# Performance work log

Hardware: AMD Instinct MI355X
Metric: run time of the kernel (lower is better)

## Reference

```python
import jax, jax.numpy as jnp
import numpy as np

B, S, D, H, E, F, K = 4, 1024, 1024, 16, 8, 4096, 2
HD = D // H  # 64
EPS = 1e-6


def _rmsnorm(x, w):
    return x * jax.lax.rsqrt(jnp.mean(x * x, axis=-1, keepdims=True) + EPS) * w


def _rope(x, cos, sin):
    # x: [B,S,H,HD]; cos/sin: [S,HD//2]
    b, s, h, hd = x.shape
    x2 = x.reshape(b, s, h, hd // 2, 2)
    xr, xi = x2[..., 0], x2[..., 1]
    c = cos[None, :, None, :]
    sn = sin[None, :, None, :]
    or_ = xr * c - xi * sn
    oi = xr * sn + xi * c
    return jnp.stack([or_, oi], axis=-1).reshape(b, s, h, hd)


def setup_inputs() -> dict:
    key = jax.random.key(0)
    ks = jax.random.split(key, 16)
    sc = 0.02
    # rotary tables (standard LLaMa rope)
    inv = 1.0 / (10000.0 ** (np.arange(0, HD, 2, dtype=np.float32) / HD))
    ang = np.outer(np.arange(S, dtype=np.float32), inv)
    return {
        "q": jax.random.normal(ks[0], (B, S, D), jnp.float32),
        "k": jax.random.normal(ks[1], (B, S, D), jnp.float32),
        "v": jax.random.normal(ks[2], (B, S, D), jnp.float32),
        "freqs_cos": jnp.asarray(np.cos(ang)),
        "freqs_sin": jnp.asarray(np.sin(ang)),
        "att_norm_w": jnp.ones((D,), jnp.float32),
        "ffn_norm_w": jnp.ones((D,), jnp.float32),
        "wq": jax.random.normal(ks[3], (D, D), jnp.float32) * sc,
        "wk": jax.random.normal(ks[4], (D, D), jnp.float32) * sc,
        "wv": jax.random.normal(ks[5], (D, D), jnp.float32) * sc,
        "wo": jax.random.normal(ks[6], (D, D), jnp.float32) * sc,
        "router_w": jax.random.normal(ks[7], (E, D), jnp.float32) * sc,
        "router_b": jnp.zeros((E,), jnp.float32),
        "w1": jax.random.normal(ks[8], (E, F, D), jnp.float32) * sc,
        "w2": jax.random.normal(ks[9], (E, D, F), jnp.float32) * sc,
        "w3": jax.random.normal(ks[10], (E, F, D), jnp.float32) * sc,
        "is_causal": 1,
    }


def _attention(qn, kn, vn, freqs_cos, freqs_sin, wq, wk, wv, wo, is_causal):
    b, s, d = qn.shape
    qh = (qn @ wq.T).reshape(b, s, H, HD)
    kh = (kn @ wk.T).reshape(b, s, H, HD)
    vh = (vn @ wv.T).reshape(b, s, H, HD)
    qh = _rope(qh, freqs_cos, freqs_sin)
    kh = _rope(kh, freqs_cos, freqs_sin)
    scores = jnp.einsum("bqhd,bkhd->bhqk", qh, kh) / jnp.sqrt(jnp.float32(HD))
    if is_causal:
        causal = jnp.tril(jnp.ones((s, s), bool))
        scores = jnp.where(causal[None, None], scores, jnp.float32(-1e30))
    probs = jax.nn.softmax(scores, axis=-1)
    out = jnp.einsum("bhqk,bkhd->bqhd", probs, vh).reshape(b, s, d)
    return out @ wo.T


def _sparse_moe(x, router_w, router_b, w1, w2, w3):
    # x: [B,S,D]
    flat = x.reshape(-1, x.shape[-1])  # [T,D]
    logits = flat @ router_w.T + router_b  # [T,E]
    top_v, top_i = jax.lax.top_k(logits, K)  # eval mode: no noise
    probs = jax.nn.softmax(top_v, axis=-1)  # softmax over -inf-filled == softmax over top-k
    gates = jnp.sum(jax.nn.one_hot(top_i, E, dtype=flat.dtype) * probs[..., None], axis=1)  # [T,E]
    y = jnp.zeros_like(flat)
    for e in range(E):  # fixed small expert loop; gate==0 for unselected tokens (faithful to masked dispatch)
        hgate = jax.nn.silu(flat @ w1[e].T) * (flat @ w3[e].T)  # SwiGLU FFN_LLaMa
        y = y + gates[:, e : e + 1] * (hgate @ w2[e].T)
    return y.reshape(x.shape)


def reference(q, k, v, freqs_cos, freqs_sin, att_norm_w, ffn_norm_w, wq, wk, wv, wo,
              router_w, router_b, w1, w2, w3, is_causal):
    qn = _rmsnorm(q, att_norm_w)
    # self-attention path: k = v = normed q (q.clone())
    h = q + _attention(qn, qn, qn, freqs_cos, freqs_sin, wq, wk, wv, wo, is_causal)
    out = h + _sparse_moe(_rmsnorm(h, ffn_norm_w), router_w, router_b, w1, w2, w3)
    return out
```

## Files before the change

### kernel.cpp

```cpp
#include <hip/hip_runtime.h>
#include <hip/hip_bf16.h>
#include <math.h>

#define NB 4
#define SQ 1024
#define DM 1024
#define NH 16
#define HDm 64
#define NE 8
#define FFd 4096
#define NTOK 4096
#define RTOT 9216
#define EPSF 1e-6f

typedef __attribute__((ext_vector_type(8))) short bf16x8_t;
typedef __attribute__((ext_vector_type(4))) float f32x4_t;
typedef const __attribute__((address_space(1))) void* gas_t;
typedef __attribute__((address_space(3))) void* las_t;

__device__ __forceinline__ float b2f(unsigned short u){
  return __uint_as_float(((unsigned int)u) << 16);
}
__device__ __forceinline__ unsigned short f2b(float f){
  __hip_bfloat16 h = __float2bfloat16(f);
  unsigned short u;
  __builtin_memcpy(&u, &h, 2);
  return u;
}

__global__ __launch_bounds__(256) void convert_k(const float* __restrict__ s,
                                                 unsigned short* __restrict__ d, int n4){
  int i = blockIdx.x*256 + threadIdx.x;
  if (i >= n4) return;
  float4 v = ((const float4*)s)[i];
  ushort4 o; o.x=f2b(v.x); o.y=f2b(v.y); o.z=f2b(v.z); o.w=f2b(v.w);
  ((ushort4*)d)[i] = o;
}

__global__ __launch_bounds__(256) void split_k(const float* __restrict__ s,
                                               unsigned short* __restrict__ hi,
                                               unsigned short* __restrict__ lo, int n4){
  int i = blockIdx.x*256 + threadIdx.x;
  if (i >= n4) return;
  float4 v = ((const float4*)s)[i];
  ushort4 h, l;
  h.x=f2b(v.x); l.x=f2b(v.x - b2f(h.x));
  h.y=f2b(v.y); l.y=f2b(v.y - b2f(h.y));
  h.z=f2b(v.z); l.z=f2b(v.z - b2f(h.z));
  h.w=f2b(v.w); l.w=f2b(v.w - b2f(h.w));
  ((ushort4*)hi)[i] = h;
  ((ushort4*)lo)[i] = l;
}

__global__ __launch_bounds__(256) void rmsnorm_k(const float* __restrict__ x,
                                                 const float* __restrict__ w,
                                                 float* __restrict__ o){
  int row = blockIdx.x; int t = threadIdx.x;
  float4 v = ((const float4*)(x + (size_t)row*DM))[t];
  float ss = v.x*v.x + v.y*v.y + v.z*v.z + v.w*v.w;
  #pragma unroll
  for (int d=32; d; d>>=1) ss += __shfl_down(ss, d, 64);
  __shared__ float red[4];
  int wid = t>>6, ln = t&63;
  if (ln==0) red[wid] = ss;
  __syncthreads();
  float tot = red[0]+red[1]+red[2]+red[3];
  float sc = 1.0f/sqrtf(tot*(1.0f/DM) + EPSF);
  float4 wv = ((const float4*)w)[t];
  float4 ov = { v.x*sc*wv.x, v.y*sc*wv.y, v.z*sc*wv.z, v.w*sc*wv.w };
  ((float4*)(o + (size_t)row*DM))[t] = ov;
}

__global__ __launch_bounds__(256) void rmsnorm_split_k(const float* __restrict__ x,
                                                       const float* __restrict__ w,
                                                       unsigned short* __restrict__ hi,
                                                       unsigned short* __restrict__ lo){
  int row = blockIdx.x; int t = threadIdx.x;
  float4 v = ((const float4*)(x + (size_t)row*DM))[t];
  float ss = v.x*v.x + v.y*v.y + v.z*v.z + v.w*v.w;
  #pragma unroll
  for (int d=32; d; d>>=1) ss += __shfl_down(ss, d, 64);
  __shared__ float red[4];
  int wid = t>>6, ln = t&63;
  if (ln==0) red[wid] = ss;
  __syncthreads();
  float tot = red[0]+red[1]+red[2]+red[3];
  float sc = 1.0f/sqrtf(tot*(1.0f/DM) + EPSF);
  float4 wv = ((const float4*)w)[t];
  float4 ov = { v.x*sc*wv.x, v.y*sc*wv.y, v.z*sc*wv.z, v.w*sc*wv.w };
  ushort4 h, l;
  h.x=f2b(ov.x); l.x=f2b(ov.x - b2f(h.x));
  h.y=f2b(ov.y); l.y=f2b(ov.y - b2f(h.y));
  h.z=f2b(ov.z); l.z=f2b(ov.z - b2f(h.z));
  h.w=f2b(ov.w); l.w=f2b(ov.w - b2f(h.w));
  ((ushort4*)(hi + (size_t)row*DM))[t] = h;
  ((ushort4*)(lo + (size_t)row*DM))[t] = l;
}

__global__ __launch_bounds__(256) void gemm_nt_split(
  const unsigned short* __restrict__ Ah, const unsigned short* __restrict__ Al,
  const unsigned short* __restrict__ Bh0, const unsigned short* __restrict__ Bl0,
  const unsigned short* __restrict__ Bh1, const unsigned short* __restrict__ Bl1,
  const unsigned short* __restrict__ Bh2, const unsigned short* __restrict__ Bl2,
  float* __restrict__ C0, float* __restrict__ C1, float* __restrict__ C2,
  const float* __restrict__ resid, int Kd, int Ncols)
{
  const unsigned short* Bh = (blockIdx.z==0)?Bh0:(blockIdx.z==1)?Bh1:Bh2;
  const unsigned short* Bl = (blockIdx.z==0)?Bl0:(blockIdx.z==1)?Bl1:Bl2;
  float* C = (blockIdx.z==0)?C0:(blockIdx.z==1)?C1:C2;
  __shared__ unsigned short AsH[128*32];
  __shared__ unsigned short AsL[128*32];
  __shared__ unsigned short BsH[128*32];
  __shared__ unsigned short BsL[128*32];
  const int t = threadIdx.x;
  const int w = t>>6, lane = t&63;
  const int wm = w>>1, wn = w&1;
  const int lm = lane&15, fk = (lane>>4)*8;
  const int row0 = blockIdx.y*128, col0 = blockIdx.x*128;
  f32x4_t acc[4][4];
  #pragma unroll
  for (int i=0;i<4;i++)
    #pragma unroll
    for (int j=0;j<4;j++){ f32x4_t z = {0.f,0.f,0.f,0.f}; acc[i][j]=z; }
  for (int k0=0;k0<Kd;k0+=32){
    __syncthreads();
    #pragma unroll
    for (int j=0;j<2;j++){
      const int chunk = j*4 + w;
      const int gt = chunk*64 + lane;
      const int rw_ = gt>>2, kp = (gt&3)*8;
      const size_t aoff = (size_t)(row0+rw_)*Kd + k0 + kp;
      const size_t boff = (size_t)(col0+rw_)*Kd + k0 + kp;
      __builtin_amdgcn_global_load_lds((gas_t)(Ah + aoff), (las_t)(AsH + chunk*512), 16, 0, 0);
      __builtin_amdgcn_global_load_lds((gas_t)(Al + aoff), (las_t)(AsL + chunk*512), 16, 0, 0);
      __builtin_amdgcn_global_load_lds((gas_t)(Bh + boff), (las_t)(BsH + chunk*512), 16, 0, 0);
      __builtin_amdgcn_global_load_lds((gas_t)(Bl + boff), (las_t)(BsL + chunk*512), 16, 0, 0);
    }
    __syncthreads();
    bf16x8_t ah[4], al[4], bh[4], bl[4];
    #pragma unroll
    for (int f=0;f<4;f++){
      const size_t ao = (size_t)(wm*64 + f*16 + lm)*32 + fk;
      const size_t bo = (size_t)(wn*64 + f*16 + lm)*32 + fk;
      ah[f] = *(const bf16x8_t*)(AsH + ao);
      al[f] = *(const bf16x8_t*)(AsL + ao);
      bh[f] = *(const bf16x8_t*)(BsH + bo);
      bl[f] = *(const bf16x8_t*)(BsL + bo);
    }
    #pragma unroll
    for (int i=0;i<4;i++)
      #pragma unroll
      for (int j=0;j<4;j++){
        acc[i][j] = __builtin_amdgcn_mfma_f32_16x16x32_bf16(ah[i], bh[j], acc[i][j], 0, 0, 0);
        acc[i][j] = __builtin_amdgcn_mfma_f32_16x16x32_bf16(al[i], bh[j], acc[i][j], 0, 0, 0);
        acc[i][j] = __builtin_amdgcn_mfma_f32_16x16x32_bf16(ah[i], bl[j], acc[i][j], 0, 0, 0);
      }
  }
  const int rbase = row0 + wm*64 + (lane>>4)*4;
  const int cbase = col0 + wn*64 + lm;
  #pragma unroll
  for (int i=0;i<4;i++)
    #pragma unroll
    for (int j=0;j<4;j++)
      #pragma unroll
      for (int r=0;r<4;r++){
        const size_t idx = (size_t)(rbase + i*16 + r)*Ncols + cbase + j*16;
        float v = acc[i][j][r];
        if (resid) v += resid[idx];
        C[idx] = v;
      }
}

__global__ __launch_bounds__(256) void rope_bf16_k(const float* __restrict__ qh,
  const float* __restrict__ kh, const float* __restrict__ fc, const float* __restrict__ fs,
  unsigned short* __restrict__ qb, unsigned short* __restrict__ kb){
  int idx = blockIdx.x*256 + threadIdx.x;
  if (idx >= NTOK*NH*32) return;
  int i = idx & 31;
  int h = (idx>>5) & (NH-1);
  int n = idx >> 9;
  int s = n & (SQ-1);
  float c = fc[s*32+i], sn = fs[s*32+i];
  size_t base = (size_t)n*DM + h*HDm + 2*i;
  float xr = qh[base], xi = qh[base+1];
  float or_ = (xr*c - xi*sn) * 0.125f;
  float oi  = (xr*sn + xi*c) * 0.125f;
  unsigned int pq = (unsigned int)f2b(or_) | ((unsigned int)f2b(oi) << 16);
  *(unsigned int*)(qb + base) = pq;
  xr = kh[base]; xi = kh[base+1];
  or_ = xr*c - xi*sn; oi = xr*sn + xi*c;
  unsigned int pk = (unsigned int)f2b(or_) | ((unsigned int)f2b(oi) << 16);
  *(unsigned int*)(kb + base) = pk;
}

__global__ __launch_bounds__(256) void vtrans_k(const float* __restrict__ vh,
                                                unsigned short* __restrict__ vT){
  __shared__ unsigned short Lt[64][72];
  const int st = blockIdx.x, bh = blockIdx.y;
  const int b = bh >> 4, h = bh & 15;
  const int t = threadIdx.x;
  const int s0 = st*64;
  const int sr = t >> 2, hq = (t & 3) * 16;
  const float* src = vh + ((size_t)(b*SQ + s0 + sr))*DM + h*HDm + hq;
  #pragma unroll
  for (int i=0;i<4;i++){
    float4 v = *(const float4*)(src + 4*i);
    Lt[hq+4*i+0][sr] = f2b(v.x);
    Lt[hq+4*i+1][sr] = f2b(v.y);
    Lt[hq+4*i+2][sr] = f2b(v.z);
    Lt[hq+4*i+3][sr] = f2b(v.w);
  }
  __syncthreads();
  const int hd = t >> 2, sq = (t & 3) * 16;
  unsigned short* dst = vT + ((size_t)bh*HDm + hd)*SQ + s0 + sq;
  #pragma unroll
  for (int i=0;i<2;i++){
    bf16x8_t x = *(const bf16x8_t*)&Lt[hd][sq + 8*i];
    *(bf16x8_t*)(dst + 8*i) = x;
  }
}

__global__ __launch_bounds__(256) void flash_mfma_k(
  const unsigned short* __restrict__ qb, const unsigned short* __restrict__ kb,
  const unsigned short* __restrict__ vT,
  unsigned short* __restrict__ ctxh, unsigned short* __restrict__ ctxl,
  const int* __restrict__ causp)
{
  __shared__ unsigned short Qs[2*64*32];
  __shared__ unsigned short Ks[2*64*32];
  __shared__ unsigned short Vt[2*64*32];
  __shared__ unsigned short Ps[2*64*32];
  const int qt = blockIdx.x;
  const int bh = blockIdx.y;
  const int b = bh >> 4, h = bh & 15;
  const int t = threadIdx.x;
  const int w = t >> 6, lane = t & 63;
  const int lm = lane & 15, g = lane >> 4, fk = g * 8;
  const int q0 = qt * 64;
  const size_t qkoff = (size_t)b * SQ * DM + (size_t)h * HDm;
  const size_t voff  = ((size_t)bh * HDm) * SQ;

  #pragma unroll
  for (int j=0;j<2;j++){
    const int s = j*4 + w;
    const int c = s >> 2, r0 = (s & 3) * 16;
    const int row = r0 + (lane >> 2), kp = (lane & 3) * 8;
    __builtin_amdgcn_global_load_lds((gas_t)(qb + qkoff + (size_t)(q0+row)*DM + c*32 + kp),
                                     (las_t)(Qs + s*512), 16, 0, 0);
  }
  __syncthreads();
  bf16x8_t aq0 = *(const bf16x8_t*)(Qs + 0*2048 + (w*16+lm)*32 + fk);
  bf16x8_t aq1 = *(const bf16x8_t*)(Qs + 1*2048 + (w*16+lm)*32 + fk);

  const int causal = *causp;
  const int ktmax = causal ? qt : (SQ/64 - 1);
  f32x4_t O[4];
  #pragma unroll
  for (int j=0;j<4;j++){ f32x4_t z={0.f,0.f,0.f,0.f}; O[j]=z; }
  float mrow[4], lrow[4];
  #pragma unroll
  for (int r=0;r<4;r++){ mrow[r] = -3e30f; lrow[r] = 0.f; }

  for (int kt=0; kt<=ktmax; ++kt){
    const int k0 = kt*64;
    __syncthreads();
    #pragma unroll
    for (int j=0;j<2;j++){
      const int s = j*4 + w;
      const int c = s >> 2, r0 = (s & 3) * 16;
      const int row = r0 + (lane >> 2), kp = (lane & 3) * 8;
      __builtin_amdgcn_global_load_lds((gas_t)(kb + qkoff + (size_t)(k0+row)*DM + c*32 + kp),
                                       (las_t)(Ks + s*512), 16, 0, 0);
      __builtin_amdgcn_global_load_lds((gas_t)(vT + voff + (size_t)row*SQ + k0 + c*32 + kp),
                                       (las_t)(Vt + s*512), 16, 0, 0);
    }
    __syncthreads();

    f32x4_t Sv[4];
    #pragma unroll
    for (int j=0;j<4;j++){ f32x4_t z={0.f,0.f,0.f,0.f}; Sv[j]=z; }
    #pragma unroll
    for (int j=0;j<4;j++){
      bf16x8_t b0 = *(const bf16x8_t*)(Ks + 0*2048 + (j*16+lm)*32 + fk);
      bf16x8_t b1 = *(const bf16x8_t*)(Ks + 1*2048 + (j*16+lm)*32 + fk);
      Sv[j] = __builtin_amdgcn_mfma_f32_16x16x32_bf16(aq0, b0, Sv[j], 0, 0, 0);
      Sv[j] = __builtin_amdgcn_mfma_f32_16x16x32_bf16(aq1, b1, Sv[j], 0, 0, 0);
    }
    const int rowq = q0 + w*16 + g*4;
    if (causal && kt == qt){
      #pragma unroll
      for (int j=0;j<4;j++){
        const int col = k0 + j*16 + lm;
        #pragma unroll
        for (int r=0;r<4;r++)
          if (col > rowq + r) Sv[j][r] = -3e30f;
      }
    }
    float alpha[4];
    #pragma unroll
    for (int r=0;r<4;r++){
      float m_ = fmaxf(fmaxf(Sv[0][r],Sv[1][r]), fmaxf(Sv[2][r],Sv[3][r]));
      #pragma unroll
      for (int d=1; d<16; d<<=1) m_ = fmaxf(m_, __shfl_xor(m_, d, 64));
      const float mn = fmaxf(mrow[r], m_);
      alpha[r] = __expf(mrow[r] - mn);
      mrow[r] = mn;
    }
    #pragma unroll
    for (int r=0;r<4;r++){
      const int qrow = w*16 + g*4 + r;
      float rs = 0.f;
      #pragma unroll
      for (int j=0;j<4;j++){
        const float p = __expf(Sv[j][r] - mrow[r]);
        rs += p;
        const int key5 = (((j&1)<<4) | lm) ^ (g<<3);
        Ps[(j>>1)*2048 + qrow*32 + key5] = f2b(p);
      }
      #pragma unroll
      for (int d=1; d<16; d<<=1) rs += __shfl_xor(rs, d, 64);
      lrow[r] = lrow[r]*alpha[r] + rs;
      #pragma unroll
      for (int j=0;j<4;j++) O[j][r] *= alpha[r];
    }
    const int fkp = fk ^ (((lm>>2)&3)<<3);
    bf16x8_t pa0 = *(const bf16x8_t*)(Ps + 0*2048 + (w*16+lm)*32 + fkp);
    bf16x8_t pa1 = *(const bf16x8_t*)(Ps + 1*2048 + (w*16+lm)*32 + fkp);
    #pragma unroll
    for (int j=0;j<4;j++){
      bf16x8_t v0 = *(const bf16x8_t*)(Vt + 0*2048 + (j*16+lm)*32 + fk);
      bf16x8_t v1 = *(const bf16x8_t*)(Vt + 1*2048 + (j*16+lm)*32 + fk);
      O[j] = __builtin_amdgcn_mfma_f32_16x16x32_bf16(pa0, v0, O[j], 0, 0, 0);
      O[j] = __builtin_amdgcn_mfma_f32_16x16x32_bf16(pa1, v1, O[j], 0, 0, 0);
    }
  }
  #pragma unroll
  for (int r=0;r<4;r++){
    const float il = 1.0f / lrow[r];
    const size_t rowtok = (size_t)(q0 + w*16 + g*4 + r);
    #pragma unroll
    for (int j=0;j<4;j++){
      const float v = O[j][r] * il;
      const unsigned short hi = f2b(v);
      const float lo = v - b2f(hi);
      const size_t idx = qkoff + rowtok*DM + j*16 + lm;
      ctxh[idx] = hi;
      ctxl[idx] = f2b(lo);
    }
  }
}

__global__ __launch_bounds__(256) void router_k(
  const float* __restrict__ hn, const float* __restrict__ rw, const float* __restrict__ rb,
  int* __restrict__ topi, float* __restrict__ topp, int* __restrict__ counts)
{
  const int n = blockIdx.x, t = threadIdx.x;
  float4 x = ((const float4*)(hn + (size_t)n*DM))[t];
  float p[NE];
  #pragma unroll
  for (int e=0;e<NE;e++){
    float4 wv = ((const float4*)(rw + (size_t)e*DM))[t];
    p[e] = x.x*wv.x + x.y*wv.y + x.z*wv.z + x.w*wv.w;
  }
  #pragma unroll
  for (int e=0;e<NE;e++)
    #pragma unroll
    for (int d=32; d; d>>=1) p[e] += __shfl_down(p[e], d, 64);
  __shared__ float red[4][NE];
  int wid=t>>6, ln=t&63;
  if (ln==0){
    #pragma unroll
    for (int e=0;e<NE;e++) red[wid][e]=p[e];
  }
  __syncthreads();
  if (t==0){
    float v1=-3e30f, v2=-3e30f; int i1=0, i2=0;
    for (int e=0;e<NE;e++){
      float v = red[0][e]+red[1][e]+red[2][e]+red[3][e]+rb[e];
      if (v > v1){ v2=v1;i2=i1; v1=v;i1=e; }
      else if (v > v2){ v2=v;i2=e; }
    }
    float ex = expf(v2-v1);
    float g1 = 1.0f/(1.0f+ex);
    float g2 = ex*g1;
    topi[2*n]=i1; topi[2*n+1]=i2;
    topp[2*n]=g1; topp[2*n+1]=g2;
    atomicAdd(&counts[i1],1); atomicAdd(&counts[i2],1);
  }
}

__global__ void offsets_k(const int* __restrict__ counts, int* __restrict__ offs){
  if (blockIdx.x==0 && threadIdx.x==0){
    int run=0;
    for (int e=0;e<NE;e++){ offs[e]=run; run += (counts[e]+127)&~127; }
    offs[NE]=run;
  }
}

__global__ __launch_bounds__(256) void assign_k(const int* __restrict__ topi,
  const int* __restrict__ offs, int* __restrict__ cursor,
  int* __restrict__ list, int* __restrict__ inv){
  int t = blockIdx.x*256 + threadIdx.x;
  if (t >= NTOK*2) return;
  int e = topi[t];
  int slot = atomicAdd(&cursor[e], 1);
  int pos = offs[e] + slot;
  list[pos] = t>>1;
  inv[t] = pos;
}

__global__ __launch_bounds__(256) void gather_k(const float* __restrict__ hn,
  const int* __restrict__ offs, const int* __restrict__ counts, const int* __restrict__ list,
  unsigned short* __restrict__ xg){
  const int p = blockIdx.x;
  if (p >= offs[NE]) return;
  int e=0;
  while (offs[e+1] <= p) ++e;
  const int t = threadIdx.x;
  ushort4 o;
  if (p - offs[e] < counts[e]){
    int n = list[p];
    float4 x = ((const float4*)(hn + (size_t)n*DM))[t];
    o.x=f2b(x.x); o.y=f2b(x.y); o.z=f2b(x.z); o.w=f2b(x.w);
  } else { o.x=0; o.y=0; o.z=0; o.w=0; }
  ((ushort4*)(xg + (size_t)p*DM))[t] = o;
}

__global__ __launch_bounds__(256) void gemm_moe_bf16(
  const unsigned short* __restrict__ Aall, const unsigned short* __restrict__ Wall,
  unsigned short* __restrict__ Call, const int* __restrict__ offs, int Kd, int Ncols)
{
  const int row0 = blockIdx.y*128;
  if (row0 >= offs[NE]) return;
  int e=0;
  while (offs[e+1] <= row0) ++e;
  const unsigned short* Wp = Wall + (size_t)e*Ncols*Kd;
  const int col0 = blockIdx.x*128;
  __shared__ unsigned short As[128*32];
  __shared__ unsigned short Bs[128*32];
  const int t = threadIdx.x;
  const int w = t>>6, lane = t&63;
  const int wm = w>>1, wn = w&1;
  const int lm = lane&15, fk = (lane>>4)*8;
  f32x4_t acc[4][4];
  #pragma unroll
  for (int i=0;i<4;i++)
    #pragma unroll
    for (int j=0;j<4;j++){ f32x4_t z = {0.f,0.f,0.f,0.f}; acc[i][j]=z; }
  for (int k0=0;k0<Kd;k0+=32){
    __syncthreads();
    #pragma unroll
    for (int j=0;j<2;j++){
      const int chunk = j*4 + w;
      const int gt = chunk*64 + lane;
      const int rw_ = gt>>2, kp = (gt&3)*8;
      __builtin_amdgcn_global_load_lds((gas_t)(Aall + (size_t)(row0+rw_)*Kd + k0 + kp),
                                       (las_t)(As + chunk*512), 16, 0, 0);
      __builtin_amdgcn_global_load_lds((gas_t)(Wp + (size_t)(col0+rw_)*Kd + k0 + kp),
                                       (las_t)(Bs + chunk*512), 16, 0, 0);
    }
    __syncthreads();
    bf16x8_t af[4], bfr[4];
    #pragma unroll
    for (int f=0;f<4;f++){
      af[f]  = *(const bf16x8_t*)(As + (size_t)(wm*64 + f*16 + lm)*32 + fk);
      bfr[f] = *(const bf16x8_t*)(Bs + (size_t)(wn*64 + f*16 + lm)*32 + fk);
    }
    #pragma unroll
    for (int i=0;i<4;i++)
      #pragma unroll
      for (int j=0;j<4;j++)
        acc[i][j] = __builtin_amdgcn_mfma_f32_16x16x32_bf16(af[i], bfr[j], acc[i][j], 0, 0, 0);
  }
  const int rbase = row0 + wm*64 + (lane>>4)*4;
  const int cbase = col0 + wn*64 + lm;
  #pragma unroll
  for (int i=0;i<4;i++)
    #pragma unroll
    for (int j=0;j<4;j++)
      #pragma unroll
      for (int r=0;r<4;r++)
        Call[(size_t)(rbase + i*16 + r)*Ncols + cbase + j*16] = f2b(acc[i][j][r]);
}

__global__ __launch_bounds__(256) void silu_mul_k(unsigned short* __restrict__ h1,
                                                  const unsigned short* __restrict__ h3){
  size_t i = (size_t)blockIdx.x*256 + threadIdx.x;
  ushort4 a = ((const ushort4*)h1)[i];
  ushort4 b = ((const ushort4*)h3)[i];
  ushort4 o;
  float fa, fb, s_;
  fa=b2f(a.x); fb=b2f(b.x); s_=fa/(1.f+__expf(-fa)); o.x=f2b(s_*fb);
  fa=b2f(a.y); fb=b2f(b.y); s_=fa/(1.f+__expf(-fa)); o.y=f2b(s_*fb);
  fa=b2f(a.z); fb=b2f(b.z); s_=fa/(1.f+__expf(-fa)); o.z=f2b(s_*fb);
  fa=b2f(a.w); fb=b2f(b.w); s_=fa/(1.f+__expf(-fa)); o.w=f2b(s_*fb);
  ((ushort4*)h1)[i] = o;
}

__global__ __launch_bounds__(256) void combine_k(const float* __restrict__ h,
  const unsigned short* __restrict__ yb, const float* __restrict__ topp,
  const int* __restrict__ inv, float* __restrict__ out)
{
  const int n = blockIdx.x, t = threadIdx.x;
  const int p0 = inv[2*n], p1 = inv[2*n+1];
  const float g0 = topp[2*n], g1 = topp[2*n+1];
  float4 hv = ((const float4*)(h + (size_t)n*DM))[t];
  ushort4 y0 = ((const ushort4*)(yb + (size_t)p0*DM))[t];
  ushort4 y1 = ((const ushort4*)(yb + (size_t)p1*DM))[t];
  float4 ov;
  ov.x = hv.x + g0*b2f(y0.x) + g1*b2f(y1.x);
  ov.y = hv.y + g0*b2f(y0.y) + g1*b2f(y1.y);
  ov.z = hv.z + g0*b2f(y0.z) + g1*b2f(y1.z);
  ov.w = hv.w + g0*b2f(y0.w) + g1*b2f(y1.w);
  ((float4*)(out + (size_t)n*DM))[t] = ov;
}

extern "C" void kernel_launch(void* const* d_in, const int* in_sizes, int n_in,
                              void* d_out, int out_size, void* d_ws, size_t ws_size,
                              hipStream_t stream)
{
  (void)in_sizes; (void)n_in; (void)out_size; (void)ws_size;
  const float* q    = (const float*)d_in[0];
  const float* fc   = (const float*)d_in[3];
  const float* fs   = (const float*)d_in[4];
  const float* attw = (const float*)d_in[5];
  const float* ffnw = (const float*)d_in[6];
  const float* wq   = (const float*)d_in[7];
  const float* wk   = (const float*)d_in[8];
  const float* wv   = (const float*)d_in[9];
  const float* wo   = (const float*)d_in[10];
  const float* rw   = (const float*)d_in[11];
  const float* rb   = (const float*)d_in[12];
  const float* w1   = (const float*)d_in[13];
  const float* w2   = (const float*)d_in[14];
  const float* w3   = (const float*)d_in[15];
  const int*   caus = (const int*)d_in[16];
  float* out = (float*)d_out;

  char* ws = (char*)d_ws;
  size_t off = 0;
  auto take = [&](size_t bytes)->char*{ char* r = ws + off; off += (bytes + 255) & ~(size_t)255; return r; };
  unsigned short* qnh = (unsigned short*)take((size_t)NTOK*DM*2);
  unsigned short* qnl = (unsigned short*)take((size_t)NTOK*DM*2);
  float* qh   = (float*)take((size_t)NTOK*DM*4);
  float* kh   = (float*)take((size_t)NTOK*DM*4);
  float* vh   = (float*)take((size_t)NTOK*DM*4);
  float* hbuf = (float*)take((size_t)NTOK*DM*4);
  unsigned short* h1  = (unsigned short*)take((size_t)RTOT*FFd*2);
  unsigned short* h3  = (unsigned short*)take((size_t)RTOT*FFd*2);
  unsigned short* yb  = (unsigned short*)take((size_t)RTOT*DM*2);
  unsigned short* w1b = (unsigned short*)take((size_t)NE*FFd*DM*2);
  unsigned short* w3b = (unsigned short*)take((size_t)NE*FFd*DM*2);
  unsigned short* w2b = (unsigned short*)take((size_t)NE*FFd*DM*2);
  int*   counts = (int*)take(64);
  int*   cursor = counts + 8;
  int*   offs   = (int*)take(64);
  int*   topi   = (int*)take((size_t)NTOK*2*4);
  float* topp   = (float*)take((size_t)NTOK*2*4);
  int*   list   = (int*)take((size_t)RTOT*4);
  int*   inv    = (int*)take((size_t)NTOK*2*4);

  unsigned short* ctxh = qnh;
  unsigned short* ctxl = qnl;
  float* hn = kh;
  unsigned short* xg = yb;
  unsigned short* wqh = (unsigned short*)h1;
  unsigned short* wql = wqh + (size_t)DM*DM;
  unsigned short* wkh = wql + (size_t)DM*DM;
  unsigned short* wkl = wkh + (size_t)DM*DM;
  unsigned short* wvh = wkl + (size_t)DM*DM;
  unsigned short* wvl = wvh + (size_t)DM*DM;
  unsigned short* woh = wvl + (size_t)DM*DM;
  unsigned short* wol = woh + (size_t)DM*DM;
  unsigned short* qb  = wqh + 8*(size_t)DM*DM;
  unsigned short* kb  = qb + (size_t)NTOK*DM;
  unsigned short* vTb = (unsigned short*)h3;

  const int nw4 = NE*FFd*DM/4;
  convert_k<<<nw4/256, 256, 0, stream>>>(w1, w1b, nw4);
  convert_k<<<nw4/256, 256, 0, stream>>>(w3, w3b, nw4);
  convert_k<<<nw4/256, 256, 0, stream>>>(w2, w2b, nw4);

  const int nwq4 = DM*DM/4;
  split_k<<<nwq4/256, 256, 0, stream>>>(wq, wqh, wql, nwq4);
  split_k<<<nwq4/256, 256, 0, stream>>>(wk, wkh, wkl, nwq4);
  split_k<<<nwq4/256, 256, 0, stream>>>(wv, wvh, wvl, nwq4);
  split_k<<<nwq4/256, 256, 0, stream>>>(wo, woh, wol, nwq4);

  rmsnorm_split_k<<<NTOK, 256, 0, stream>>>(q, attw, qnh, qnl);
  gemm_nt_split<<<dim3(8,32,3), 256, 0, stream>>>(qnh, qnl,
      wqh, wql, wkh, wkl, wvh, wvl, qh, kh, vh, nullptr, DM, DM);
  rope_bf16_k<<<NTOK*NH*32/256, 256, 0, stream>>>(qh, kh, fc, fs, qb, kb);
  vtrans_k<<<dim3(SQ/64, NB*NH), 256, 0, stream>>>(vh, vTb);
  flash_mfma_k<<<dim3(SQ/64, NB*NH), 256, 0, stream>>>(qb, kb, vTb, ctxh, ctxl, caus);
  gemm_nt_split<<<dim3(8,32,1), 256, 0, stream>>>(ctxh, ctxl,
      woh, wol, woh, wol, woh, wol, hbuf, hbuf, hbuf, q, DM, DM);
  rmsnorm_k<<<NTOK, 256, 0, stream>>>(hbuf, ffnw, hn);

  hipMemsetAsync(counts, 0, 64, stream);
  router_k<<<NTOK, 256, 0, stream>>>(hn, rw, rb, topi, topp, counts);
  offsets_k<<<1, 64, 0, stream>>>(counts, offs);
  assign_k<<<NTOK*2/256, 256, 0, stream>>>(topi, offs, cursor, list, inv);
  gather_k<<<RTOT, 256, 0, stream>>>(hn, offs, counts, list, xg);

  gemm_moe_bf16<<<dim3(FFd/128, RTOT/128), 256, 0, stream>>>(xg, w1b, h1, offs, DM, FFd);
  gemm_moe_bf16<<<dim3(FFd/128, RTOT/128), 256, 0, stream>>>(xg, w3b, h3, offs, DM, FFd);
  silu_mul_k<<<RTOT*FFd/4/256, 256, 0, stream>>>(h1, h3);
  gemm_moe_bf16<<<dim3(DM/128, RTOT/128), 256, 0, stream>>>(h1, w2b, yb, offs, FFd, DM);
  combine_k<<<NTOK, 256, 0, stream>>>(hbuf, yb, topp, inv, out);
}
```

Before: 1.219 ms.

## Retile MoE GEMM to 256x256 with double-buffered swizzled LDS

Rewrites the grouped expert GEMM to use 256x256 output tiles with 512 threads, a K-step of 64, double-buffered LDS staging that overlaps global loads with MFMA, an XOR swizzle against bank conflicts, a workgroup remap for locality, and setprio around the MFMA block. Expert padding grows to multiples of 256, which raises the padded row total and adds some wasted compute on padding rows. The goal is more data reuse per load and fewer idle cycles waiting on memory in the three dominant FFN GEMMs.

```diff
diff --git a/kernel.cpp b/kernel.cpp
--- a/kernel.cpp
+++ b/kernel.cpp
@@ -10,7 +10,7 @@
 #define NE 8
 #define FFd 4096
 #define NTOK 4096
-#define RTOT 9216
+#define RTOT 10240
 #define EPSF 1e-6f
 
 typedef __attribute__((ext_vector_type(8))) short bf16x8_t;
@@ -392,7 +392,7 @@
 __global__ void offsets_k(const int* __restrict__ counts, int* __restrict__ offs){
   if (blockIdx.x==0 && threadIdx.x==0){
     int run=0;
-    for (int e=0;e<NE;e++){ offs[e]=run; run += (counts[e]+127)&~127; }
+    for (int e=0;e<NE;e++){ offs[e]=run; run += (counts[e]+255)&~255; }
     offs[NE]=run;
   }
 }
@@ -426,61 +426,94 @@
   ((ushort4*)(xg + (size_t)p*DM))[t] = o;
 }
 
-__global__ __launch_bounds__(256) void gemm_moe_bf16(
+__global__ __launch_bounds__(512, 2) void gemm_moe_bf16(
   const unsigned short* __restrict__ Aall, const unsigned short* __restrict__ Wall,
   unsigned short* __restrict__ Call, const int* __restrict__ offs, int Kd, int Ncols)
 {
-  const int row0 = blockIdx.y*128;
+  __shared__ unsigned short As[2*256*64];
+  __shared__ unsigned short Bs[2*256*64];
+  const int Gx = gridDim.x;
+  const int nwg = Gx * gridDim.y;
+  const int orig = blockIdx.y * Gx + blockIdx.x;
+  const int wg = (orig & 7) * (nwg >> 3) + (orig >> 3);
+  const int ry = wg / Gx, cx = wg - ry*Gx;
+  const int row0 = ry * 256;
   if (row0 >= offs[NE]) return;
-  int e=0;
+  int e = 0;
   while (offs[e+1] <= row0) ++e;
-  const unsigned short* Wp = Wall + (size_t)e*Ncols*Kd;
-  const int col0 = blockIdx.x*128;
-  __shared__ unsigned short As[128*32];
-  __shared__ unsigned short Bs[128*32];
+  const unsigned short* Wp = Wall + (size_t)e * Ncols * Kd;
+  const int col0 = cx * 256;
+
   const int t = threadIdx.x;
-  const int w = t>>6, lane = t&63;
-  const int wm = w>>1, wn = w&1;
-  const int lm = lane&15, fk = (lane>>4)*8;
-  f32x4_t acc[4][4];
-  #pragma unroll
-  for (int i=0;i<4;i++)
-    #pragma unroll
-    for (int j=0;j<4;j++){ f32x4_t z = {0.f,0.f,0.f,0.f}; acc[i][j]=z; }
-  for (int k0=0;k0<Kd;k0+=32){
+  const int w = t >> 6, lane = t & 63;
+  const int wm = w >> 2, wn = w & 3;
+  const int lm = lane & 15, g = lane >> 4;
+  const int lsub = lane >> 3;
+  const int scol = (((lane & 7) ^ lsub) << 3);
+  const int swzr = (lm & 7) << 4;
+
+  f32x4_t acc[8][4];
+  #pragma unroll
+  for (int i=0;i<8;i++)
+    #pragma unroll
+    for (int j=0;j<4;j++){ f32x4_t z={0.f,0.f,0.f,0.f}; acc[i][j]=z; }
+
+  const int KT = Kd >> 6;
+  auto stage = [&](int buf, int k0){
+    #pragma unroll
+    for (int j=0;j<4;j++){
+      const int s = j*8 + w;
+      const int rl = s*8 + lsub;
+      __builtin_amdgcn_global_load_lds(
+        (gas_t)(Aall + (size_t)(row0+rl)*Kd + k0 + scol),
+        (las_t)(As + buf*16384 + s*512), 16, 0, 0);
+      __builtin_amdgcn_global_load_lds(
+        (gas_t)(Wp + (size_t)(col0+rl)*Kd + k0 + scol),
+        (las_t)(Bs + buf*16384 + s*512), 16, 0, 0);
+    }
+  };
+
+  stage(0, 0);
+  __syncthreads();
+  int cur = 0;
+  for (int kt=0; kt<KT; ++kt){
+    if (kt+1 < KT) stage(cur^1, (kt+1)<<6);
+    const unsigned short* Ab = As + cur*16384;
+    const unsigned short* Bb = Bs + cur*16384;
+    #pragma unroll
+    for (int half=0; half<2; ++half){
+      const int cb = (half<<6) | (g<<4);
+      const int co = (cb ^ swzr) >> 1;
+      bf16x8_t a[8], bfr[4];
+      #pragma unroll
+      for (int f=0;f<8;f++)
+        a[f] = *(const bf16x8_t*)(Ab + (wm*128 + f*16 + lm)*64 + co);
+      #pragma unroll
+      for (int j=0;j<4;j++)
+        bfr[j] = *(const bf16x8_t*)(Bb + (wn*64 + j*16 + lm)*64 + co);
+      __builtin_amdgcn_s_setprio(1);
+      #pragma unroll
+      for (int i=0;i<8;i++)
+        #pragma unroll
+        for (int j=0;j<4;j++)
+          acc[i][j] = __builtin_amdgcn_mfma_f32_16x16x32_bf16(a[i], bfr[j], acc[i][j], 0, 0, 0);
+      __builtin_amdgcn_s_setprio(0);
+    }
     __syncthreads();
-    #pragma unroll
-    for (int j=0;j<2;j++){
-      const int chunk = j*4 + w;
-      const int gt = chunk*64 + lane;
-      const int rw_ = gt>>2, kp = (gt&3)*8;
-      __builtin_amdgcn_global_load_lds((gas_t)(Aall + (size_t)(row0+rw_)*Kd + k0 + kp),
-                                       (las_t)(As + chunk*512), 16, 0, 0);
-      __builtin_amdgcn_global_load_lds((gas_t)(Wp + (size_t)(col0+rw_)*Kd + k0 + kp),
-                                       (las_t)(Bs + chunk*512), 16, 0, 0);
-    }
-    __syncthreads();
-    bf16x8_t af[4], bfr[4];
-    #pragma unroll
-    for (int f=0;f<4;f++){
-      af[f]  = *(const bf16x8_t*)(As + (size_t)(wm*64 + f*16 + lm)*32 + fk);
-      bfr[f] = *(const bf16x8_t*)(Bs + (size_t)(wn*64 + f*16 + lm)*32 + fk);
-    }
-    #pragma unroll
-    for (int i=0;i<4;i++)
-      #pragma unroll
-      for (int j=0;j<4;j++)
-        acc[i][j] = __builtin_amdgcn_mfma_f32_16x16x32_bf16(af[i], bfr[j], acc[i][j], 0, 0, 0);
-  }
-  const int rbase = row0 + wm*64 + (lane>>4)*4;
-  const int cbase = col0 + wn*64 + lm;
-  #pragma unroll
-  for (int i=0;i<4;i++)
-    #pragma unroll
-    for (int j=0;j<4;j++)
+    cur ^= 1;
+  }
+
+  #pragma unroll
+  for (int i=0;i<8;i++){
+    const int grow = row0 + wm*128 + i*16 + g*4;
+    #pragma unroll
+    for (int j=0;j<4;j++){
+      const int gcol = col0 + wn*64 + j*16 + lm;
       #pragma unroll
       for (int r=0;r<4;r++)
-        Call[(size_t)(rbase + i*16 + r)*Ncols + cbase + j*16] = f2b(acc[i][j][r]);
+        Call[(size_t)(grow + r)*Ncols + gcol] = f2b(acc[i][j][r]);
+    }
+  }
 }
 
 __global__ __launch_bounds__(256) void silu_mul_k(unsigned short* __restrict__ h1,
@@ -603,9 +636,9 @@
   assign_k<<<NTOK*2/256, 256, 0, stream>>>(topi, offs, cursor, list, inv);
   gather_k<<<RTOT, 256, 0, stream>>>(hn, offs, counts, list, xg);
 
-  gemm_moe_bf16<<<dim3(FFd/128, RTOT/128), 256, 0, stream>>>(xg, w1b, h1, offs, DM, FFd);
-  gemm_moe_bf16<<<dim3(FFd/128, RTOT/128), 256, 0, stream>>>(xg, w3b, h3, offs, DM, FFd);
+  gemm_moe_bf16<<<dim3(FFd/256, RTOT/256), 512, 0, stream>>>(xg, w1b, h1, offs, DM, FFd);
+  gemm_moe_bf16<<<dim3(FFd/256, RTOT/256), 512, 0, stream>>>(xg, w3b, h3, offs, DM, FFd);
   silu_mul_k<<<RTOT*FFd/4/256, 256, 0, stream>>>(h1, h3);
-  gemm_moe_bf16<<<dim3(DM/128, RTOT/128), 256, 0, stream>>>(h1, w2b, yb, offs, FFd, DM);
+  gemm_moe_bf16<<<dim3(DM/256, RTOT/256), 512, 0, stream>>>(h1, w2b, yb, offs, FFd, DM);
   combine_k<<<NTOK, 256, 0, stream>>>(hbuf, yb, topp, inv, out);
 }
```

Result: no change. 1.216 ms (-0.2%).
